# Kernel tuning notes

Hardware: AMD Instinct MI355X
Metric: run time of the kernel (lower is better)

The kernel has to match this reference:

```python
import jax, jax.numpy as jnp
import numpy as np

N = 100000


def seg_mean(feat, src, dst, n):
    # gather at src, scatter-mean at dst (PyG mean aggr: 0 for isolated nodes)
    s = jax.ops.segment_sum(feat[src], dst, num_segments=n)
    cnt = jax.ops.segment_sum(jnp.ones((src.shape[0],), feat.dtype), dst, num_segments=n)
    return s / jnp.maximum(cnt, 1.0)[:, None]


def setup_inputs() -> dict:
    key = jax.random.key(0)
    ks = jax.random.split(key, 8)
    d_in, d_h = 64, 32
    E = 1_250_000
    inp = {
        "x": jax.random.normal(ks[0], (N, d_in), jnp.float32),
        "W1_pos": jax.random.normal(ks[1], (2 * d_in, d_h), jnp.float32) * 0.05,
        "b1_pos": jnp.zeros((d_h,), jnp.float32),
        "W1_neg": jax.random.normal(ks[2], (2 * d_in, d_h), jnp.float32) * 0.05,
        "b1_neg": jnp.zeros((d_h,), jnp.float32),
        "W2_pos": jax.random.normal(ks[3], (3 * d_h, d_h), jnp.float32) * 0.05,
        "b2_pos": jnp.zeros((d_h,), jnp.float32),
        "W2_neg": jax.random.normal(ks[4], (3 * d_h, d_h), jnp.float32) * 0.05,
        "b2_neg": jnp.zeros((d_h,), jnp.float32),
        "pos_edge_index": jax.random.randint(ks[5], (2, E), 0, N, jnp.int64),
        "neg_edge_index": jax.random.randint(ks[6], (2, E), 0, N, jnp.int64),
    }
    return inp


def reference(x, W1_pos, b1_pos, W1_neg, b1_neg, W2_pos, b2_pos, W2_neg, b2_neg,
              pos_edge_index, neg_edge_index):
    ps, pd = pos_edge_index[0], pos_edge_index[1]
    ns, nd = neg_edge_index[0], neg_edge_index[1]
    n = x.shape[0]

    # --- layer 1 (first_aggr=True) ---
    ap = seg_mean(x, ps, pd, n)          # [N, 64]
    an = seg_mean(x, ns, nd, n)
    out_p = jnp.concatenate([ap, x], -1) @ W1_pos + b1_pos   # [N, 32]
    out_n = jnp.concatenate([an, x], -1) @ W1_neg + b1_neg
    z = jnp.tanh(jnp.concatenate([out_p, out_n], -1))        # [N, 64]

    # --- layer 2 (first_aggr=False) ---
    d_h = out_p.shape[-1]
    zp, zn = z[:, :d_h], z[:, d_h:]
    out_p = jnp.concatenate([seg_mean(zp, ps, pd, n), seg_mean(zn, ns, nd, n), zp], -1) @ W2_pos + b2_pos
    out_n = jnp.concatenate([seg_mean(zn, ps, pd, n), seg_mean(zp, ns, nd, n), zn], -1) @ W2_neg + b2_neg
    z = jnp.tanh(jnp.concatenate([out_p, out_n], -1))
    return z
```

## Files before the change

### kernel.cpp

```cpp
#include <hip/hip_runtime.h>
#include <math.h>


typedef _Float16 h4 __attribute__((ext_vector_type(4)));
typedef _Float16 h8 __attribute__((ext_vector_type(8)));
typedef float f32x4 __attribute__((ext_vector_type(4)));

__device__ inline h8 shflx8(h8 v, int m) {
    int4 i = __builtin_bit_cast(int4, v);
    i.x = __shfl_xor(i.x, m);
    i.y = __shfl_xor(i.y, m);
    i.z = __shfl_xor(i.z, m);
    i.w = __shfl_xor(i.w, m);
    return __builtin_bit_cast(h8, i);
}

__device__ inline float fast_tanh(float v) {
    float e = __expf(2.0f * v);
    return 1.0f - 2.0f / (e + 1.0f);
}


#define BSHIFT 9
#define BSIZE  512
#define NBMAX  512
#define CAP    8192


__device__ inline float b1map(const float* W1p, const float* W1n, int k, int c)
{
    if (c < 32) {
        if (k < 64)   return W1p[k * 32 + c];
        if (k >= 128) return W1p[(k - 64) * 32 + c];
        return 0.0f;
    } else {
        int cn = c - 32;
        if (k >= 64)  return W1n[(k - 64) * 32 + cn];
        return 0.0f;
    }
}

__device__ inline float b2map(const float* W2p, const float* W2n, int k, int c)
{
    if (c < 32) {
        if (k < 32)               return W2p[k * 32 + c];
        if (k >= 96 && k < 128)   return W2p[(k - 96 + 32) * 32 + c];
        if (k >= 128 && k < 160)  return W2p[(k - 128 + 64) * 32 + c];
        return 0.0f;
    } else {
        int cn = c - 32;
        if (k >= 32 && k < 64)    return W2n[(k - 32) * 32 + cn];
        if (k >= 64 && k < 96)    return W2n[(k - 64 + 32) * 32 + cn];
        if (k >= 160)             return W2n[(k - 160 + 64) * 32 + cn];
        return 0.0f;
    }
}


__global__ void __launch_bounds__(256) mega_k(
    const int* __restrict__ pos, const int* __restrict__ neg,
    int* __restrict__ pcnt, unsigned* __restrict__ ebuf,
    int E, int n, int nb, int bblocks,
    const float4* __restrict__ x, h4* __restrict__ xh, int n4, int cvtBlocks,
    const float* __restrict__ W1p, const float* __restrict__ W1n,
    const float* __restrict__ W2p, const float* __restrict__ W2n,
    _Float16* __restrict__ Bpack)
{
    int tid = threadIdx.x;
    int bid = blockIdx.x;

    if (bid >= bblocks) {
        int cb = bid - bblocks;
        if (cb < cvtBlocks) {
            int i = cb * 256 + tid;
            if (i < n4) {
                float4 v = x[i];
                h4 o = { (_Float16)v.x, (_Float16)v.y, (_Float16)v.z, (_Float16)v.w };
                xh[i] = o;
            }
        } else {
            int slot = (cb - cvtBlocks) * 256 + tid;
            if (slot < 2 * 24 * 64) {
                int mat  = slot / (24 * 64);
                int rem  = slot % (24 * 64);
                int fg   = rem / 64;
                int lane = rem % 64;
                int kk = fg >> 2, nt = fg & 3;
                int g = lane >> 4, m = lane & 15;
                _Float16* dst = Bpack + (size_t)slot * 8;
                int c = nt * 16 + m;
                #pragma unroll
                for (int j = 0; j < 8; ++j) {
                    int k = kk * 32 + g * 8 + j;
                    float v = mat ? b2map(W2p, W2n, k, c) : b1map(W1p, W1n, k, c);
                    dst[j] = (_Float16)v;
                }
            }
        }
        return;
    }

    __shared__ int cnt[NBMAX], gbase[NBMAX];
    const int K = 32;
    int base = bid * (256 * K);

    for (int i = tid; i < nb; i += 256) cnt[i] = 0;
    __syncthreads();

    unsigned val[K], pr[K];
    #pragma unroll
    for (int k = 0; k < K; ++k) {
        int e = base + k * 256 + tid;
        pr[k] = 0xFFFFFFFFu;
        if (e < 2 * E) {
            int nd, sr;
            if (e < E) { nd = pos[E + e];                 sr = pos[e]; }
            else       { int ee = e - E; nd = n + neg[E + ee]; sr = neg[ee]; }
            int p = nd >> BSHIFT;
            val[k] = ((unsigned)(nd & (BSIZE - 1)) << 17) | (unsigned)sr;
            int rank = atomicAdd(&cnt[p], 1);
            pr[k] = ((unsigned)p << 13) | (unsigned)rank;
        }
    }
    __syncthreads();
    for (int i = tid; i < nb; i += 256) {
        int c = cnt[i];
        gbase[i] = c ? atomicAdd(&pcnt[i], c) : 0;
    }
    __syncthreads();
    #pragma unroll
    for (int k = 0; k < K; ++k) {
        if (pr[k] != 0xFFFFFFFFu) {
            int p = (int)(pr[k] >> 13);
            int off = gbase[p] + (int)(pr[k] & 0x1FFFu);
            if (off < CAP) ebuf[(size_t)p * CAP + off] = val[k];
        }
    }
}

__global__ void __launch_bounds__(256) scatter_k(
    const unsigned* __restrict__ ebuf, const int* __restrict__ pcnt,
    int* __restrict__ cur, int* __restrict__ col, int n, int nb)
{
    __shared__ int lcnt[BSIZE], lbase[BSIZE], sc[256], bb[NBMAX];
    __shared__ int lcol[CAP];
    int p = blockIdx.x;
    int tid = threadIdx.x;
    int n2 = 2 * n;
    int lo = p << BSHIFT;
    int nn = min(BSIZE, n2 - lo);
    int cnt = min(pcnt[p], CAP);
    const unsigned* buf = ebuf + (size_t)p * CAP;

    {
        int a0 = (2 * tid     < nb) ? pcnt[2 * tid]     : 0;
        int a1 = (2 * tid + 1 < nb) ? pcnt[2 * tid + 1] : 0;
        int s = a0 + a1;
        sc[tid] = s;
        __syncthreads();
        for (int off = 1; off < 256; off <<= 1) {
            int t = (tid >= off) ? sc[tid - off] : 0;
            __syncthreads();
            sc[tid] += t;
            __syncthreads();
        }
        int excl = sc[tid] - s;
        bb[2 * tid] = excl;
        bb[2 * tid + 1] = excl + a0;
    }

    lcnt[tid] = 0; lcnt[tid + 256] = 0;
    __syncthreads();
    for (int i = tid; i < cnt; i += 256) {
        unsigned v = buf[i];
        atomicAdd(&lcnt[v >> 17], 1);
    }
    __syncthreads();
    int a0 = lcnt[2 * tid], a1 = lcnt[2 * tid + 1];
    int s = a0 + a1;
    sc[tid] = s;
    __syncthreads();
    for (int off = 1; off < 256; off <<= 1) {
        int t = (tid >= off) ? sc[tid - off] : 0;
        __syncthreads();
        sc[tid] += t;
        __syncthreads();
    }
    int excl = sc[tid] - s;
    lbase[2 * tid] = excl;
    lbase[2 * tid + 1] = excl + a0;
    __syncthreads();
    int gb = bb[p];
    for (int i = tid; i < nn; i += 256)
        cur[lo + i] = gb + lbase[i] + lcnt[i];
    __syncthreads();
    for (int i = tid; i < cnt; i += 256) {
        unsigned v = buf[i];
        int rel = (int)(v >> 17);
        int slot = atomicAdd(&lbase[rel], 1);
        lcol[slot] = (int)(v & 0x1FFFFu);
    }
    __syncthreads();
    for (int t = tid; t < cnt; t += 256)
        col[gb + t] = lcol[t];
}


__global__ void __launch_bounds__(256) agg_k(
    const h8* __restrict__ feat8,
    const int* __restrict__ cur, const int* __restrict__ col,
    h8* __restrict__ ag8, int n)
{
    int tid = threadIdx.x;
    int wave = tid >> 6, lane = tid & 63;
    int s = lane >> 2, f = lane & 3;
    int list = s >> 3;
    int sub = s & 7;

    int stride = gridDim.x * 4;
    for (int node = blockIdx.x * 4 + wave; node < n; node += stride) {
        int idx = list ? n + node : node;
        int r0 = idx ? cur[idx - 1] : 0;
        int r1 = cur[idx];

        h8 acc0 = {}, acc1 = {};
        #pragma unroll 2
        for (int it = r0 + sub; it < r1; it += 8) {
            unsigned srcb = (unsigned)col[it] * 8;
            acc0 = acc0 + feat8[srcb + f];
            acc1 = acc1 + feat8[srcb + 4 + f];
        }
        acc0 = acc0 + shflx8(acc0, 4);
        acc1 = acc1 + shflx8(acc1, 4);
        acc0 = acc0 + shflx8(acc0, 8);
        acc1 = acc1 + shflx8(acc1, 8);
        acc0 = acc0 + shflx8(acc0, 16);
        acc1 = acc1 + shflx8(acc1, 16);
        _Float16 inv = (_Float16)(1.0f / (float)max(r1 - r0, 1));
        h8 iv = { inv, inv, inv, inv, inv, inv, inv, inv };
        if (sub == 0) {
            ag8[(unsigned)(node * 16 + list * 8 + f)]     = acc0 * iv;
            ag8[(unsigned)(node * 16 + list * 8 + 4 + f)] = acc1 * iv;
        }
    }
}


#define ROWP 200

__global__ void __launch_bounds__(256) gemm_k(
    const h8* __restrict__ ag8, const h8* __restrict__ feat8,
    const h8* __restrict__ Bp,
    const float* __restrict__ bp, const float* __restrict__ bn,
    float* __restrict__ outf, _Float16* __restrict__ outh,
    int f32out, int n)
{
    __shared__ _Float16 A_lds[64 * ROWP];
    int tid = threadIdx.x;
    int base = blockIdx.x * 64;

    for (int ch = tid; ch < 64 * 24; ch += 256) {
        int r = ch / 24, p = ch % 24;
        int row = min(base + r, n - 1);
        h8 v = (p < 16) ? ag8[(size_t)row * 16 + p]
                        : feat8[(size_t)row * 8 + (p - 16)];
        *(h8*)&A_lds[r * ROWP + p * 8] = v;
    }
    __syncthreads();

    int w = tid >> 6, lane = tid & 63;
    int m = lane & 15, g = lane >> 4;

    h8 a[6];
    #pragma unroll
    for (int kk = 0; kk < 6; ++kk)
        a[kk] = *(const h8*)&A_lds[(w * 16 + m) * ROWP + kk * 32 + g * 8];

    #pragma unroll
    for (int nt = 0; nt < 4; ++nt) {
        f32x4 acc = { 0.f, 0.f, 0.f, 0.f };
        #pragma unroll
        for (int kk = 0; kk < 6; ++kk) {
            h8 b = Bp[(kk * 4 + nt) * 64 + lane];
            acc = __builtin_amdgcn_mfma_f32_16x16x32_f16(a[kk], b, acc, 0, 0, 0);
        }
        int colc = nt * 16 + m;
        float bias = (colc < 32) ? bp[colc] : bn[colc - 32];
        #pragma unroll
        for (int reg = 0; reg < 4; ++reg) {
            int node = base + w * 16 + g * 4 + reg;
            if (node < n) {
                float val = fast_tanh(acc[reg] + bias);
                if (f32out) outf[(size_t)node * 64 + colc] = val;
                else        outh[(size_t)node * 64 + colc] = (_Float16)val;
            }
        }
    }
}

extern "C" void kernel_launch(void* const* d_in, const int* in_sizes, int n_in,
                              void* d_out, int out_size, void* d_ws, size_t ws_size,
                              hipStream_t stream)
{
    const float* x   = (const float*)d_in[0];
    const float* W1p = (const float*)d_in[1];
    const float* b1p = (const float*)d_in[2];
    const float* W1n = (const float*)d_in[3];
    const float* b1n = (const float*)d_in[4];
    const float* W2p = (const float*)d_in[5];
    const float* b2p = (const float*)d_in[6];
    const float* W2n = (const float*)d_in[7];
    const float* b2n = (const float*)d_in[8];
    const int*   pos = (const int*)d_in[9];
    const int*   neg = (const int*)d_in[10];

    int n = in_sizes[0] / 64;
    int E = in_sizes[9] / 2;
    int n2 = 2 * n;
    int nb = (n2 + BSIZE - 1) / BSIZE;

    int*      pcnt  = (int*)d_ws;
    int*      cur   = pcnt + NBMAX;
    int*      col   = cur + n2;
    _Float16* Bpack = (_Float16*)(col + 2 * (size_t)E);
    _Float16* xh    = Bpack + 2 * 24 * 64 * 8;
    unsigned* ebuf  = (unsigned*)(xh + (size_t)n * 64);
    _Float16* zh    = (_Float16*)ebuf;
    h8*       ag8   = (h8*)d_out;

    hipMemsetAsync(pcnt, 0, NBMAX * sizeof(int), stream);

    int bblocks = (2 * E + 8191) / 8192;
    int n4 = n * 16;
    int cvtBlocks = (n4 + 255) / 256;

    mega_k<<<bblocks + cvtBlocks + 12, 256, 0, stream>>>(
        pos, neg, pcnt, ebuf, E, n, nb, bblocks,
        (const float4*)x, (h4*)xh, n4, cvtBlocks,
        W1p, W1n, W2p, W2n, Bpack);

    scatter_k<<<nb, 256, 0, stream>>>(ebuf, pcnt, cur, col, n, nb);

    int ablocks = 2048;
    int gblocks = (n + 63) / 64;

    agg_k <<<ablocks, 256, 0, stream>>>((const h8*)xh, cur, col, ag8, n);
    gemm_k<<<gblocks, 256, 0, stream>>>(ag8, (const h8*)xh, (const h8*)Bpack,
                                        b1p, b1n, nullptr, zh, 0, n);

    agg_k <<<ablocks, 256, 0, stream>>>((const h8*)zh, cur, col, ag8, n);
    gemm_k<<<gblocks, 256, 0, stream>>>(ag8, (const h8*)zh,
                                        (const h8*)(Bpack + 24 * 64 * 8),
                                        b2p, b2n, (float*)d_out, nullptr, 1, n);
}
```

Baseline: 274.5 us.

## Two-pass bucketing with fixed grid, grid-stride convert, and 512-thread scatter

The edge-bucketing kernel moves from a fixed 32-edges-per-thread register pass with one block per 8192 edges to a fixed 1024-block grid. Each block first counts over its edge range, reserves global space, then re-reads the edges and writes them using a second round of shared atomics. The x-to-half conversion becomes grid-stride over 512 blocks, and scatter_k runs with 512 threads per block. The aim is to cut the register pressure from holding 64 values per thread and to improve occupancy. The cost is reading the edge indices twice and doing twice as many shared atomics.

After: 277.9 us. Within noise of the previous version (+1.2%).

```diff
diff --git a/kernel.cpp b/kernel.cpp
--- a/kernel.cpp
+++ b/kernel.cpp
@@ -72,8 +72,8 @@
     if (bid >= bblocks) {
         int cb = bid - bblocks;
         if (cb < cvtBlocks) {
-            int i = cb * 256 + tid;
-            if (i < n4) {
+            int gs = cvtBlocks * 256;
+            for (int i = cb * 256 + tid; i < n4; i += gs) {
                 float4 v = x[i];
                 h4 o = { (_Float16)v.x, (_Float16)v.y, (_Float16)v.z, (_Float16)v.w };
                 xh[i] = o;
@@ -101,44 +101,37 @@
     }
 
     __shared__ int cnt[NBMAX], gbase[NBMAX];
-    const int K = 32;
-    int base = bid * (256 * K);
+    int per = (2 * E + bblocks - 1) / bblocks;
+    int e0 = bid * per;
+    int e1 = min(e0 + per, 2 * E);
 
     for (int i = tid; i < nb; i += 256) cnt[i] = 0;
     __syncthreads();
 
-    unsigned val[K], pr[K];
-    #pragma unroll
-    for (int k = 0; k < K; ++k) {
-        int e = base + k * 256 + tid;
-        pr[k] = 0xFFFFFFFFu;
-        if (e < 2 * E) {
-            int nd, sr;
-            if (e < E) { nd = pos[E + e];                 sr = pos[e]; }
-            else       { int ee = e - E; nd = n + neg[E + ee]; sr = neg[ee]; }
-            int p = nd >> BSHIFT;
-            val[k] = ((unsigned)(nd & (BSIZE - 1)) << 17) | (unsigned)sr;
-            int rank = atomicAdd(&cnt[p], 1);
-            pr[k] = ((unsigned)p << 13) | (unsigned)rank;
-        }
+    for (int e = e0 + tid; e < e1; e += 256) {
+        int nd = (e < E) ? pos[E + e] : n + neg[E + (e - E)];
+        atomicAdd(&cnt[nd >> BSHIFT], 1);
     }
     __syncthreads();
     for (int i = tid; i < nb; i += 256) {
         int c = cnt[i];
         gbase[i] = c ? atomicAdd(&pcnt[i], c) : 0;
-    }
-    __syncthreads();
-    #pragma unroll
-    for (int k = 0; k < K; ++k) {
-        if (pr[k] != 0xFFFFFFFFu) {
-            int p = (int)(pr[k] >> 13);
-            int off = gbase[p] + (int)(pr[k] & 0x1FFFu);
-            if (off < CAP) ebuf[(size_t)p * CAP + off] = val[k];
-        }
-    }
-}
-
-__global__ void __launch_bounds__(256) scatter_k(
+        cnt[i] = 0;
+    }
+    __syncthreads();
+    for (int e = e0 + tid; e < e1; e += 256) {
+        int nd, sr;
+        if (e < E) { nd = pos[E + e];                 sr = pos[e]; }
+        else       { int ee = e - E; nd = n + neg[E + ee]; sr = neg[ee]; }
+        int p = nd >> BSHIFT;
+        int r = gbase[p] + atomicAdd(&cnt[p], 1);
+        if (r < CAP)
+            ebuf[(size_t)p * CAP + r] =
+                ((unsigned)(nd & (BSIZE - 1)) << 17) | (unsigned)sr;
+    }
+}
+
+__global__ void __launch_bounds__(512) scatter_k(
     const unsigned* __restrict__ ebuf, const int* __restrict__ pcnt,
     int* __restrict__ cur, int* __restrict__ col, int n, int nb)
 {
@@ -153,55 +146,64 @@
     const unsigned* buf = ebuf + (size_t)p * CAP;
 
     {
-        int a0 = (2 * tid     < nb) ? pcnt[2 * tid]     : 0;
-        int a1 = (2 * tid + 1 < nb) ? pcnt[2 * tid + 1] : 0;
-        int s = a0 + a1;
-        sc[tid] = s;
+        int a0 = 0, a1 = 0, s = 0;
+        if (tid < 256) {
+            a0 = (2 * tid     < nb) ? pcnt[2 * tid]     : 0;
+            a1 = (2 * tid + 1 < nb) ? pcnt[2 * tid + 1] : 0;
+            s = a0 + a1;
+            sc[tid] = s;
+        }
         __syncthreads();
         for (int off = 1; off < 256; off <<= 1) {
-            int t = (tid >= off) ? sc[tid - off] : 0;
+            int t = (tid < 256 && tid >= off) ? sc[tid - off] : 0;
             __syncthreads();
-            sc[tid] += t;
+            if (tid < 256) sc[tid] += t;
             __syncthreads();
         }
-        int excl = sc[tid] - s;
-        bb[2 * tid] = excl;
-        bb[2 * tid + 1] = excl + a0;
-    }
-
-    lcnt[tid] = 0; lcnt[tid + 256] = 0;
-    __syncthreads();
-    for (int i = tid; i < cnt; i += 256) {
+        if (tid < 256) {
+            int excl = sc[tid] - s;
+            bb[2 * tid]     = excl;
+            bb[2 * tid + 1] = excl + a0;
+        }
+    }
+
+    for (int i = tid; i < BSIZE; i += 512) lcnt[i] = 0;
+    __syncthreads();
+    for (int i = tid; i < cnt; i += 512)
+        atomicAdd(&lcnt[buf[i] >> 17], 1);
+    __syncthreads();
+    {
+        int a0 = 0, a1 = 0, s = 0;
+        if (tid < 256) {
+            a0 = lcnt[2 * tid]; a1 = lcnt[2 * tid + 1];
+            s = a0 + a1;
+            sc[tid] = s;
+        }
+        __syncthreads();
+        for (int off = 1; off < 256; off <<= 1) {
+            int t = (tid < 256 && tid >= off) ? sc[tid - off] : 0;
+            __syncthreads();
+            if (tid < 256) sc[tid] += t;
+            __syncthreads();
+        }
+        if (tid < 256) {
+            int excl = sc[tid] - s;
+            lbase[2 * tid]     = excl;
+            lbase[2 * tid + 1] = excl + a0;
+        }
+    }
+    __syncthreads();
+    int gb = bb[p];
+    for (int i = tid; i < nn; i += 512)
+        cur[lo + i] = gb + lbase[i] + lcnt[i];
+    __syncthreads();
+    for (int i = tid; i < cnt; i += 512) {
         unsigned v = buf[i];
-        atomicAdd(&lcnt[v >> 17], 1);
-    }
-    __syncthreads();
-    int a0 = lcnt[2 * tid], a1 = lcnt[2 * tid + 1];
-    int s = a0 + a1;
-    sc[tid] = s;
-    __syncthreads();
-    for (int off = 1; off < 256; off <<= 1) {
-        int t = (tid >= off) ? sc[tid - off] : 0;
-        __syncthreads();
-        sc[tid] += t;
-        __syncthreads();
-    }
-    int excl = sc[tid] - s;
-    lbase[2 * tid] = excl;
-    lbase[2 * tid + 1] = excl + a0;
-    __syncthreads();
-    int gb = bb[p];
-    for (int i = tid; i < nn; i += 256)
-        cur[lo + i] = gb + lbase[i] + lcnt[i];
-    __syncthreads();
-    for (int i = tid; i < cnt; i += 256) {
-        unsigned v = buf[i];
-        int rel = (int)(v >> 17);
-        int slot = atomicAdd(&lbase[rel], 1);
+        int slot = atomicAdd(&lbase[v >> 17], 1);
         lcol[slot] = (int)(v & 0x1FFFFu);
     }
     __syncthreads();
-    for (int t = tid; t < cnt; t += 256)
+    for (int t = tid; t < cnt; t += 512)
         col[gb + t] = lcol[t];
 }
 
@@ -330,16 +332,16 @@
 
     hipMemsetAsync(pcnt, 0, NBMAX * sizeof(int), stream);
 
-    int bblocks = (2 * E + 8191) / 8192;
+    int bblocks = 1024;
     int n4 = n * 16;
-    int cvtBlocks = (n4 + 255) / 256;
+    int cvtBlocks = 512;
 
     mega_k<<<bblocks + cvtBlocks + 12, 256, 0, stream>>>(
         pos, neg, pcnt, ebuf, E, n, nb, bblocks,
         (const float4*)x, (h4*)xh, n4, cvtBlocks,
         W1p, W1n, W2p, W2n, Bpack);
 
-    scatter_k<<<nb, 256, 0, stream>>>(ebuf, pcnt, cur, col, n, nb);
+    scatter_k<<<nb, 512, 0, stream>>>(ebuf, pcnt, cur, col, n, nb);
 
     int ablocks = 2048;
     int gblocks = (n + 63) / 64;
```
